# Kernel optimization log

Hardware: AMD Instinct MI355X
Metric: run time of the kernel (lower is better)

Reference implementation:

```python
import jax, jax.numpy as jnp
import numpy as np

MARGIN = 1.0
NUM_CLASSES = 1024


def setup_inputs() -> dict:
    key = jax.random.key(0)
    k1, k2 = jax.random.split(key)
    embeddings = jax.random.normal(k1, (8192, 128), dtype=jnp.float32)
    labels = jax.random.randint(k2, (8192,), 0, NUM_CLASSES, dtype=jnp.int64)
    return {"embeddings": embeddings, "labels": labels}


def reference(embeddings, labels):
    """Triplet loss with hard-negative mining, fully vectorized.

    Matches TripletLossWithMining(margin=1.0, mining_strategy='hard'):
      - squared-Euclidean pairwise distance matrix, relu-clamped, zero diagonal
      - for every (anchor i, positive p): hardest negative n* = argmin_{n: label!=label_i} d[i,n]
      - triplet kept iff d[i,n*] < d[i,p]; loss = mean relu(d[i,p] - d[i,n*] + margin)
    """
    B = embeddings.shape[0]
    sq = jnp.sum(embeddings * embeddings, axis=1, keepdims=True)          # [B,1]
    dist = sq + sq.T - 2.0 * (embeddings @ embeddings.T)                   # [B,B]
    dist = jax.nn.relu(dist)
    eye = jnp.eye(B, dtype=bool)
    dist = jnp.where(eye, jnp.zeros((), dist.dtype), dist)                 # fill_diagonal_(0)

    same = labels[:, None] == labels[None, :]                              # [B,B]
    pos_mask = same & ~eye
    neg_mask = ~same
    has_neg = jnp.any(neg_mask, axis=1)                                    # [B]

    # hardest (closest) negative per anchor
    neg_d = jnp.where(neg_mask, dist, jnp.array(jnp.inf, dist.dtype))
    hardest_neg = jnp.min(neg_d, axis=1)                                   # [B]

    # triplet (i,p) is kept iff p is a valid positive, i has a negative,
    # and hardest_neg[i] < pos_dist d[i,p]
    valid = pos_mask & has_neg[:, None] & (hardest_neg[:, None] < dist)    # [B,B]

    per_triplet = jax.nn.relu(dist - hardest_neg[:, None] + MARGIN)        # [B,B]
    count = jnp.sum(valid)
    total = jnp.sum(jnp.where(valid, per_triplet, jnp.zeros((), dist.dtype)))
    loss = total / jnp.maximum(count, 1).astype(dist.dtype)
    return loss, count
```

## Files before the change

### kernel.cpp

```cpp
#include <hip/hip_runtime.h>
#include <stdint.h>

#define BB 8192
#define DD 128
#define MARGIN 1.0f
#define CCAP 48
#define NBLK_POS (BB / 4)
#define NT 64
#define NCH 16
#define JTPC (NT / NCH)

typedef __attribute__((ext_vector_type(8))) short short8_t;
typedef __attribute__((ext_vector_type(4))) float f32x4;

__device__ __forceinline__ unsigned short f2bf(float f) {
  unsigned u = __float_as_uint(f);
  u = (u + 0x7fffu + ((u >> 16) & 1u)) >> 16;
  return (unsigned short)u;
}

__global__ void prep_kernel(const float* __restrict__ E, const int* __restrict__ lab,
                            unsigned short* __restrict__ Ebf,
                            float* __restrict__ sq,
                            int* __restrict__ cls_cnt, int* __restrict__ cls_idx) {
  int wid = threadIdx.x >> 6, lane = threadIdx.x & 63;
  int row = blockIdx.x * 4 + wid;
  const float2 v = *(const float2*)(E + (size_t)row * DD + lane * 2);
  ushort2 bb;
  bb.x = f2bf(v.x);
  bb.y = f2bf(v.y);
  *(ushort2*)(Ebf + (size_t)row * DD + lane * 2) = bb;
  float s = v.x * v.x + v.y * v.y;
  for (int off = 1; off < 64; off <<= 1) s += __shfl_xor(s, off);
  if (lane == 0) {
    sq[row] = s;
    int labi = lab[row];
    int p = atomicAdd(&cls_cnt[labi], 1);
    if (p < CCAP) cls_idx[labi * CCAP + p] = row;
  }
}

__global__ __launch_bounds__(256) void dist_min_kernel(
    const unsigned short* __restrict__ Ebf, const float* __restrict__ sq,
    const int* __restrict__ lab, float* __restrict__ part) {
  __shared__ __align__(16) char ldsA[128 * 256];
  __shared__ int labI[128];
  __shared__ float redMin[4][64];

  const int tid = threadIdx.x;
  const int p = blockIdx.x >> 4, c = blockIdx.x & (NCH - 1);
  const int rI = p * 128;

  for (int q = tid; q < 2048; q += 256) {
    int r = q >> 4, cc = q & 15;
    int dst = r * 256 + ((cc * 16) ^ ((r & 7) << 4));
    *(float4*)(ldsA + dst) = *(const float4*)(Ebf + (size_t)(rI + r) * DD + cc * 8);
  }
  if (tid < 128) labI[tid] = lab[rI + tid];
  __syncthreads();

  const int wid = tid >> 6, lane = tid & 63;
  const int wr = wid >> 1, wc = wid & 1;
  const int rowbase = wr * 64, colbase = wc * 64;
  const int cl = lane & 15, rg = lane >> 4;

  int il[4][4];
#pragma unroll
  for (int m = 0; m < 4; m++)
#pragma unroll
    for (int r = 0; r < 4; r++) il[m][r] = labI[rowbase + m * 16 + rg * 4 + r];

  float tm[4][4];
#pragma unroll
  for (int m = 0; m < 4; m++)
#pragma unroll
    for (int r = 0; r < 4; r++) tm[m][r] = __builtin_huge_valf();

#pragma unroll
  for (int t = 0; t < JTPC; t++) {
    const int rJ = (c * JTPC + t) * 128;

    short8_t b[4][4];
    int jl[4];
    float jh[4];
#pragma unroll
    for (int n = 0; n < 4; n++) {
      const int j = rJ + colbase + n * 16 + cl;
      const char* rowp = (const char*)Ebf + (size_t)j * 256 + rg * 16;
#pragma unroll
      for (int kk = 0; kk < 4; kk++) b[n][kk] = *(const short8_t*)(rowp + kk * 64);
      jl[n] = lab[j];
      jh[n] = 0.5f * sq[j];
    }

    f32x4 acc[4][4];
#pragma unroll
    for (int m = 0; m < 4; m++)
#pragma unroll
      for (int n = 0; n < 4; n++) acc[m][n] = (f32x4){0.f, 0.f, 0.f, 0.f};

#pragma unroll
    for (int kk = 0; kk < 4; kk++) {
      const int kb = kk * 64 + rg * 16;
      short8_t a[4];
#pragma unroll
      for (int m = 0; m < 4; m++) {
        int row = rowbase + m * 16 + cl;
        a[m] = *(const short8_t*)(ldsA + row * 256 + (kb ^ ((row & 7) << 4)));
      }
#pragma unroll
      for (int m = 0; m < 4; m++)
#pragma unroll
        for (int n = 0; n < 4; n++)
          acc[m][n] = __builtin_amdgcn_mfma_f32_16x16x32_bf16(a[m], b[n][kk], acc[m][n], 0, 0, 0);
    }

#pragma unroll
    for (int m = 0; m < 4; m++)
#pragma unroll
      for (int n = 0; n < 4; n++) {
        f32x4 v = acc[m][n];
#pragma unroll
        for (int r = 0; r < 4; r++) {
          float u = jh[n] - v[r];
          if (il[m][r] != jl[n]) tm[m][r] = fminf(tm[m][r], u);
        }
      }
  }

#pragma unroll
  for (int m = 0; m < 4; m++)
#pragma unroll
    for (int r = 0; r < 4; r++) {
      float t = tm[m][r];
      t = fminf(t, __shfl_xor(t, 1));
      t = fminf(t, __shfl_xor(t, 2));
      t = fminf(t, __shfl_xor(t, 4));
      t = fminf(t, __shfl_xor(t, 8));
      tm[m][r] = t;
    }
  if (cl == 0) {
#pragma unroll
    for (int m = 0; m < 4; m++)
#pragma unroll
      for (int r = 0; r < 4; r++) redMin[wid][m * 16 + rg * 4 + r] = tm[m][r];
  }
  __syncthreads();
  if (wc == 0) {
    float v = fminf(redMin[wid][lane], redMin[wid + 1][lane]);
    part[(size_t)c * BB + rI + rowbase + lane] = v;
  }
}

__global__ void reduce_min_kernel(const float* __restrict__ part, float* __restrict__ tmin) {
  const int row = blockIdx.x * 256 + threadIdx.x;
  float m = __builtin_huge_valf();
#pragma unroll
  for (int cch = 0; cch < NCH; cch++) m = fminf(m, part[(size_t)cch * BB + row]);
  tmin[row] = m;
}

__global__ void pos_loss_kernel(const float* __restrict__ E, const int* __restrict__ lab,
                                const float* __restrict__ sq, const float* __restrict__ tmin,
                                const int* __restrict__ cls_cnt, const int* __restrict__ cls_idx,
                                float* __restrict__ ptot, int* __restrict__ pcnt) {
  __shared__ float stot[4];
  __shared__ int scnt[4];
  const int tid = threadIdx.x, wid = tid >> 6, lane = tid & 63;
  const int i = blockIdx.x * 4 + wid;
  const int labi = lab[i];
  int n = cls_cnt[labi];
  if (n > CCAP) n = CCAP;
  const float2 ei = *(const float2*)(E + (size_t)i * DD + lane * 2);
  const float sqi = sq[i];
  const float hn = fmaxf(sqi + 2.0f * tmin[i], 0.0f);
  float tsum = 0.0f;
  int tcnt = 0;
  for (int s = 0; s < n; s++) {
    int j = cls_idx[labi * CCAP + s];
    if (j == i) continue;
    float2 ej = *(const float2*)(E + (size_t)j * DD + lane * 2);
    float pp = ei.x * ej.x + ei.y * ej.y;
    for (int off = 1; off < 64; off <<= 1) pp += __shfl_xor(pp, off);
    float d = fmaxf(sqi + sq[j] - 2.0f * pp, 0.0f);
    if (hn < d) {
      tcnt++;
      tsum += d - hn + MARGIN;
    }
  }
  if (lane == 0) {
    stot[wid] = tsum;
    scnt[wid] = tcnt;
  }
  __syncthreads();
  if (tid == 0) {
    ptot[blockIdx.x] = stot[0] + stot[1] + stot[2] + stot[3];
    pcnt[blockIdx.x] = scnt[0] + scnt[1] + scnt[2] + scnt[3];
  }
}

__global__ void finalize_kernel(const float* __restrict__ ptot, const int* __restrict__ pcnt,
                                float* __restrict__ out) {
  __shared__ float stot[4];
  __shared__ int scnt[4];
  const int tid = threadIdx.x, wid = tid >> 6, lane = tid & 63;
  float t = 0.0f;
  int c = 0;
  for (int k = tid; k < NBLK_POS; k += 256) {
    t += ptot[k];
    c += pcnt[k];
  }
  for (int off = 1; off < 64; off <<= 1) {
    t += __shfl_xor(t, off);
    c += __shfl_xor(c, off);
  }
  if (lane == 0) {
    stot[wid] = t;
    scnt[wid] = c;
  }
  __syncthreads();
  if (tid == 0) {
    float tt = stot[0] + stot[1] + stot[2] + stot[3];
    int cc = scnt[0] + scnt[1] + scnt[2] + scnt[3];
    out[0] = tt / (float)(cc > 0 ? cc : 1);
    out[1] = (float)cc;
  }
}

extern "C" void kernel_launch(void* const* d_in, const int* in_sizes, int n_in,
                              void* d_out, int out_size, void* d_ws, size_t ws_size,
                              hipStream_t stream) {
  const float* E = (const float*)d_in[0];
  const int* lab = (const int*)d_in[1];
  float* out = (float*)d_out;

  char* ws = (char*)d_ws;
  unsigned short* Ebf = (unsigned short*)ws;
  float* sq = (float*)(ws + (size_t)BB * DD * 2);
  float* tmin = (float*)((char*)sq + BB * 4);
  int* cls_cnt = (int*)((char*)tmin + BB * 4);
  int* cls_idx = (int*)((char*)cls_cnt + 1024 * 4);
  float* ptot = (float*)((char*)cls_idx + 1024 * CCAP * 4);
  int* pcnt = (int*)((char*)ptot + NBLK_POS * 4);
  float* part = (float*)((char*)pcnt + NBLK_POS * 4);

  hipMemsetAsync(cls_cnt, 0, 1024 * 4, stream);
  prep_kernel<<<BB / 4, 256, 0, stream>>>(E, lab, Ebf, sq, cls_cnt, cls_idx);
  dist_min_kernel<<<NT * NCH, 256, 0, stream>>>(Ebf, sq, lab, part);
  reduce_min_kernel<<<BB / 256, 256, 0, stream>>>(part, tmin);
  pos_loss_kernel<<<NBLK_POS, 256, 0, stream>>>(E, lab, sq, tmin, cls_cnt, cls_idx, ptot, pcnt);
  finalize_kernel<<<1, 256, 0, stream>>>(ptot, pcnt, out);
}
```

Baseline: 129.4 us.

## Stage B tiles in double-buffered LDS via global_load_lds and fold reduce into pos_loss

The distance-min kernel now streams B column tiles of 64 rows into double-buffered LDS using direct global-to-LDS loads and prefetches the next tile while computing the current one. Column labels and half-norms are staged once in LDS. The chunk count drops from 16 to 8, so each block covers 1024 columns. The separate reduce_min kernel is removed and its min over partials is folded into pos_loss. This cuts redundant global loads and one launch, but adds a barrier per tile, uses more LDS (lower occupancy), and halves the grid to 512 blocks.

```diff
diff --git a/kernel.cpp b/kernel.cpp
--- a/kernel.cpp
+++ b/kernel.cpp
@@ -6,12 +6,17 @@
 #define MARGIN 1.0f
 #define CCAP 48
 #define NBLK_POS (BB / 4)
-#define NT 64
-#define NCH 16
-#define JTPC (NT / NCH)
+#define NCH 8
+#define CHCOLS (BB / NCH)
+#define TPC (CHCOLS / 64)
 
 typedef __attribute__((ext_vector_type(8))) short short8_t;
 typedef __attribute__((ext_vector_type(4))) float f32x4;
+
+#define GLL16(g, l)                                                                   \
+  __builtin_amdgcn_global_load_lds(                                                   \
+      (const __attribute__((address_space(1))) unsigned int*)(g),                     \
+      (__attribute__((address_space(3))) unsigned int*)(l), 16, 0, 0)
 
 __device__ __forceinline__ unsigned short f2bf(float f) {
   unsigned u = __float_as_uint(f);
@@ -44,25 +49,44 @@
     const unsigned short* __restrict__ Ebf, const float* __restrict__ sq,
     const int* __restrict__ lab, float* __restrict__ part) {
   __shared__ __align__(16) char ldsA[128 * 256];
+  __shared__ __align__(16) char ldsB[2][64 * 256];
+  __shared__ int labC[CHCOLS];
+  __shared__ float hC[CHCOLS];
   __shared__ int labI[128];
   __shared__ float redMin[4][64];
 
   const int tid = threadIdx.x;
-  const int p = blockIdx.x >> 4, c = blockIdx.x & (NCH - 1);
+  const int p = blockIdx.x >> 3, c = blockIdx.x & (NCH - 1);
   const int rI = p * 128;
-
-  for (int q = tid; q < 2048; q += 256) {
-    int r = q >> 4, cc = q & 15;
-    int dst = r * 256 + ((cc * 16) ^ ((r & 7) << 4));
-    *(float4*)(ldsA + dst) = *(const float4*)(Ebf + (size_t)(rI + r) * DD + cc * 8);
+  const int cBase = c * CHCOLS;
+
+  const int wid = tid >> 6, lane = tid & 63;
+  const int l4 = lane >> 4, c16 = lane & 15;
+
+#pragma unroll
+  for (int q = 0; q < 8; q++) {
+    int r = wid * 32 + q * 4 + l4;
+    int chunk = c16 ^ (r & 7);
+    GLL16((const char*)Ebf + (size_t)(rI + r) * 256 + chunk * 16,
+          ldsA + wid * 8192 + q * 1024);
+  }
+#pragma unroll
+  for (int q = 0; q < 4; q++) {
+    int r = wid * 16 + q * 4 + l4;
+    int chunk = c16 ^ (r & 7);
+    GLL16((const char*)Ebf + (size_t)(cBase + r) * 256 + chunk * 16,
+          ldsB[0] + wid * 4096 + q * 1024);
+  }
+  for (int q = tid; q < CHCOLS; q += 256) {
+    labC[q] = lab[cBase + q];
+    hC[q] = 0.5f * sq[cBase + q];
   }
   if (tid < 128) labI[tid] = lab[rI + tid];
   __syncthreads();
 
-  const int wid = tid >> 6, lane = tid & 63;
   const int wr = wid >> 1, wc = wid & 1;
-  const int rowbase = wr * 64, colbase = wc * 64;
-  const int cl = lane & 15, rg = lane >> 4;
+  const int rowbase = wr * 64;
+  const int cl = c16, rg = l4;
 
   int il[4][4];
 #pragma unroll
@@ -76,49 +100,58 @@
 #pragma unroll
     for (int r = 0; r < 4; r++) tm[m][r] = __builtin_huge_valf();
 
-#pragma unroll
-  for (int t = 0; t < JTPC; t++) {
-    const int rJ = (c * JTPC + t) * 128;
-
-    short8_t b[4][4];
-    int jl[4];
-    float jh[4];
-#pragma unroll
-    for (int n = 0; n < 4; n++) {
-      const int j = rJ + colbase + n * 16 + cl;
-      const char* rowp = (const char*)Ebf + (size_t)j * 256 + rg * 16;
-#pragma unroll
-      for (int kk = 0; kk < 4; kk++) b[n][kk] = *(const short8_t*)(rowp + kk * 64);
-      jl[n] = lab[j];
-      jh[n] = 0.5f * sq[j];
-    }
-
-    f32x4 acc[4][4];
+  for (int t = 0; t < TPC; t++) {
+    const int cur = t & 1;
+    if (t + 1 < TPC) {
+#pragma unroll
+      for (int q = 0; q < 4; q++) {
+        int r = wid * 16 + q * 4 + l4;
+        int chunk = c16 ^ (r & 7);
+        GLL16((const char*)Ebf + (size_t)(cBase + (t + 1) * 64 + r) * 256 + chunk * 16,
+              ldsB[cur ^ 1] + wid * 4096 + q * 1024);
+      }
+    }
+
+    int jl[2];
+    float jh[2];
+#pragma unroll
+    for (int n = 0; n < 2; n++) {
+      int j = t * 64 + wc * 32 + n * 16 + cl;
+      jl[n] = labC[j];
+      jh[n] = hC[j];
+    }
+
+    f32x4 acc[4][2];
 #pragma unroll
     for (int m = 0; m < 4; m++)
 #pragma unroll
-      for (int n = 0; n < 4; n++) acc[m][n] = (f32x4){0.f, 0.f, 0.f, 0.f};
+      for (int n = 0; n < 2; n++) acc[m][n] = (f32x4){0.f, 0.f, 0.f, 0.f};
 
 #pragma unroll
     for (int kk = 0; kk < 4; kk++) {
       const int kb = kk * 64 + rg * 16;
-      short8_t a[4];
+      short8_t a[4], b[2];
 #pragma unroll
       for (int m = 0; m < 4; m++) {
         int row = rowbase + m * 16 + cl;
         a[m] = *(const short8_t*)(ldsA + row * 256 + (kb ^ ((row & 7) << 4)));
       }
 #pragma unroll
+      for (int n = 0; n < 2; n++) {
+        int row = wc * 32 + n * 16 + cl;
+        b[n] = *(const short8_t*)(ldsB[cur] + row * 256 + (kb ^ ((row & 7) << 4)));
+      }
+#pragma unroll
       for (int m = 0; m < 4; m++)
 #pragma unroll
-        for (int n = 0; n < 4; n++)
-          acc[m][n] = __builtin_amdgcn_mfma_f32_16x16x32_bf16(a[m], b[n][kk], acc[m][n], 0, 0, 0);
+        for (int n = 0; n < 2; n++)
+          acc[m][n] = __builtin_amdgcn_mfma_f32_16x16x32_bf16(a[m], b[n], acc[m][n], 0, 0, 0);
     }
 
 #pragma unroll
     for (int m = 0; m < 4; m++)
 #pragma unroll
-      for (int n = 0; n < 4; n++) {
+      for (int n = 0; n < 2; n++) {
         f32x4 v = acc[m][n];
 #pragma unroll
         for (int r = 0; r < 4; r++) {
@@ -126,6 +159,8 @@
           if (il[m][r] != jl[n]) tm[m][r] = fminf(tm[m][r], u);
         }
       }
+
+    __syncthreads();
   }
 
 #pragma unroll
@@ -152,16 +187,8 @@
   }
 }
 
-__global__ void reduce_min_kernel(const float* __restrict__ part, float* __restrict__ tmin) {
-  const int row = blockIdx.x * 256 + threadIdx.x;
-  float m = __builtin_huge_valf();
-#pragma unroll
-  for (int cch = 0; cch < NCH; cch++) m = fminf(m, part[(size_t)cch * BB + row]);
-  tmin[row] = m;
-}
-
 __global__ void pos_loss_kernel(const float* __restrict__ E, const int* __restrict__ lab,
-                                const float* __restrict__ sq, const float* __restrict__ tmin,
+                                const float* __restrict__ sq, const float* __restrict__ part,
                                 const int* __restrict__ cls_cnt, const int* __restrict__ cls_idx,
                                 float* __restrict__ ptot, int* __restrict__ pcnt) {
   __shared__ float stot[4];
@@ -173,7 +200,10 @@
   if (n > CCAP) n = CCAP;
   const float2 ei = *(const float2*)(E + (size_t)i * DD + lane * 2);
   const float sqi = sq[i];
-  const float hn = fmaxf(sqi + 2.0f * tmin[i], 0.0f);
+  float mn = __builtin_huge_valf();
+#pragma unroll
+  for (int cc = 0; cc < NCH; cc++) mn = fminf(mn, part[(size_t)cc * BB + i]);
+  const float hn = fmaxf(sqi + 2.0f * mn, 0.0f);
   float tsum = 0.0f;
   int tcnt = 0;
   for (int s = 0; s < n; s++) {
@@ -237,8 +267,7 @@
   char* ws = (char*)d_ws;
   unsigned short* Ebf = (unsigned short*)ws;
   float* sq = (float*)(ws + (size_t)BB * DD * 2);
-  float* tmin = (float*)((char*)sq + BB * 4);
-  int* cls_cnt = (int*)((char*)tmin + BB * 4);
+  int* cls_cnt = (int*)((char*)sq + BB * 4);
   int* cls_idx = (int*)((char*)cls_cnt + 1024 * 4);
   float* ptot = (float*)((char*)cls_idx + 1024 * CCAP * 4);
   int* pcnt = (int*)((char*)ptot + NBLK_POS * 4);
@@ -246,8 +275,7 @@
 
   hipMemsetAsync(cls_cnt, 0, 1024 * 4, stream);
   prep_kernel<<<BB / 4, 256, 0, stream>>>(E, lab, Ebf, sq, cls_cnt, cls_idx);
-  dist_min_kernel<<<NT * NCH, 256, 0, stream>>>(Ebf, sq, lab, part);
-  reduce_min_kernel<<<BB / 256, 256, 0, stream>>>(part, tmin);
-  pos_loss_kernel<<<NBLK_POS, 256, 0, stream>>>(E, lab, sq, tmin, cls_cnt, cls_idx, ptot, pcnt);
+  dist_min_kernel<<<64 * NCH, 256, 0, stream>>>(Ebf, sq, lab, part);
+  pos_loss_kernel<<<NBLK_POS, 256, 0, stream>>>(E, lab, sq, part, cls_cnt, cls_idx, ptot, pcnt);
   finalize_kernel<<<1, 256, 0, stream>>>(ptot, pcnt, out);
 }
```

Result: faster. 110.5 us (-14.6%).
